# Optimization experiments

Hardware: AMD Instinct MI355X
Metric: run time of the kernel (lower is better)

The kernel has to match this reference:

```python
import jax, jax.numpy as jnp
import numpy as np

H = 64  # LSTM hidden size (hardcoded in Baseline)

def _lstm_encode(x, W_ih, W_hh, b_ih, b_hh):
    # x: [N, C, T] -> final hidden state [N, H]
    # PyTorch LSTMCell gate order: i, f, g, o
    N = x.shape[0]
    xs = jnp.moveaxis(x, 2, 0)                       # [T, N, C]
    xp = jnp.einsum('tnc,gc->tng', xs, W_ih) + b_ih  # precompute input proj [T, N, 4H]
    h0 = jnp.zeros((N, H), dtype=x.dtype)
    c0 = jnp.zeros((N, H), dtype=x.dtype)

    def step(carry, xp_t):
        h, c = carry
        g = xp_t + h @ W_hh.T + b_hh                 # [N, 4H]
        i, f, gg, o = jnp.split(g, 4, axis=-1)
        c = jax.nn.sigmoid(f) * c + jax.nn.sigmoid(i) * jnp.tanh(gg)
        h = jax.nn.sigmoid(o) * jnp.tanh(c)
        return (h, c), None

    (h, _), _ = jax.lax.scan(step, (h0, c0), xp)
    return h

def _head(x, W1, b1, W2, b2, W3, b3):
    # dropout is identity at inference; relu on first two layers, none on last
    x = jax.nn.relu(x @ W1.T + b1)
    x = jax.nn.relu(x @ W2.T + b2)
    return x @ W3.T + b3

def setup_inputs() -> dict:
    key = jax.random.key(0)
    ks = jax.random.split(key, 24)
    C1, C2 = 32, 56
    N, T = 8192, 72
    d = {
        'X_obs': jax.random.normal(ks[0], (N, C1, T), jnp.float32),
        'X_wrf_cmaq': jax.random.normal(ks[1], (N, C2, T), jnp.float32),
        'obs_Wih': jax.random.normal(ks[2], (4 * H, C1), jnp.float32) * 0.1,
        'obs_Whh': jax.random.normal(ks[3], (4 * H, H), jnp.float32) * 0.1,
        'obs_bih': jax.random.normal(ks[4], (4 * H,), jnp.float32) * 0.1,
        'obs_bhh': jax.random.normal(ks[5], (4 * H,), jnp.float32) * 0.1,
        'wrf_Wih': jax.random.normal(ks[6], (4 * H, C2), jnp.float32) * 0.1,
        'wrf_Whh': jax.random.normal(ks[7], (4 * H, H), jnp.float32) * 0.1,
        'wrf_bih': jax.random.normal(ks[8], (4 * H,), jnp.float32) * 0.1,
        'wrf_bhh': jax.random.normal(ks[9], (4 * H,), jnp.float32) * 0.1,
    }
    dims = [(96, 128), (64, 96), (48, 64)]
    k = 10
    for head in ('fsp', 'o3'):
        for li, (o, i) in enumerate(dims, 1):
            d[f'{head}_W{li}'] = jax.random.normal(ks[k], (o, i), jnp.float32) * (1.0 / np.sqrt(i)); k += 1
            d[f'{head}_b{li}'] = jax.random.normal(ks[k], (o,), jnp.float32) * 0.05; k += 1
    return d

def reference(X_obs, X_wrf_cmaq,
              obs_Wih, obs_Whh, obs_bih, obs_bhh,
              wrf_Wih, wrf_Whh, wrf_bih, wrf_bhh,
              fsp_W1, fsp_b1, fsp_W2, fsp_b2, fsp_W3, fsp_b3,
              o3_W1, o3_b1, o3_W2, o3_b2, o3_W3, o3_b3):
    h_obs = _lstm_encode(X_obs, obs_Wih, obs_Whh, obs_bih, obs_bhh)
    h_wrf = _lstm_encode(X_wrf_cmaq, wrf_Wih, wrf_Whh, wrf_bih, wrf_bhh)
    feat = jnp.concatenate([h_obs, h_wrf], axis=1)  # [N, 128]
    fsp = _head(feat, fsp_W1, fsp_b1, fsp_W2, fsp_b2, fsp_W3, fsp_b3)
    o3 = _head(feat, o3_W1, o3_b1, o3_W2, o3_b2, o3_W3, o3_b3)
    return jnp.stack([fsp, o3], axis=1)  # [N, 2, 48]
```

## Files before the change

### kernel.cpp

```cpp
#include <hip/hip_runtime.h>

typedef __attribute__((ext_vector_type(8))) short short8;
typedef __attribute__((ext_vector_type(4))) float f32x4;

#define OFF_BXO   64
#define OFF_BHO   (OFF_BXO + 16384)
#define OFF_BXW   (OFF_BHO + 32768)
#define OFF_BHW   (OFF_BXW + 32768)
#define OFF_HW    (OFF_BHW + 32768)
#define OFF_BIASL (OFF_HW + 43008)
#define OFF_BIASH (OFF_BIASL + 1024)
#define OFF_FEAT  (OFF_BIASH + 832)

__device__ __forceinline__ float b2f(unsigned short u) {
    return __uint_as_float(((unsigned)u) << 16);
}
__device__ __forceinline__ unsigned short f2b(float f) {
    unsigned u = __float_as_uint(f);
    u += 0x7FFFu + ((u >> 16) & 1u);
    return (unsigned short)(u >> 16);
}
__device__ __forceinline__ float ldin(const void* p, int idx, int isf) {
    return isf ? ((const float*)p)[idx] : b2f(((const unsigned short*)p)[idx]);
}
__device__ __forceinline__ float sigmoidf_(float x) {
    return __builtin_amdgcn_rcpf(1.0f + __expf(-x));
}
__device__ __forceinline__ float tanhf_(float x) {
    return 2.0f * __builtin_amdgcn_rcpf(1.0f + __expf(-2.0f * x)) - 1.0f;
}
__device__ __forceinline__ f32x4 MFMA(short8 a, short8 b, f32x4 c) {
    return __builtin_amdgcn_mfma_f32_16x16x32_bf16(a, b, c, 0, 0, 0);
}

__global__ __launch_bounds__(256) void detect_kernel(
    const unsigned short* __restrict__ X, int* __restrict__ flag)
{
    __shared__ int cnt[256];
    int c = 0;
    for (int i = threadIdx.x; i < 2048; i += 256) {
        unsigned short u = X[2 * i];
        c += (((u >> 7) & 0xFF) >= 192);
    }
    cnt[threadIdx.x] = c;
    __syncthreads();
    if (threadIdx.x == 0) {
        int s = 0;
        for (int i = 0; i < 256; ++i) s += cnt[i];
        *flag = (s > 64) ? 1 : 0;
    }
}

__global__ __launch_bounds__(256) void prep_kernel(
    const void* oWih, const void* oWhh, const void* obih, const void* obhh,
    const void* wWih, const void* wWhh, const void* wbih, const void* wbhh,
    const void* fW1, const void* fb1, const void* fW2, const void* fb2,
    const void* fW3, const void* fb3,
    const void* oW1, const void* ob1, const void* oW2, const void* ob2,
    const void* oW3, const void* ob3,
    unsigned short* __restrict__ ws)
{
    const int isf = ((const int*)ws)[0];
    const int gid = blockIdx.x * 256 + threadIdx.x;
    const int gsz = gridDim.x * 256;

    unsigned short* BXO = ws + OFF_BXO;
    unsigned short* BHO = ws + OFF_BHO;
    unsigned short* BXW = ws + OFF_BXW;
    unsigned short* BHW = ws + OFF_BHW;
    unsigned short* HW  = ws + OFF_HW;

    for (int i = gid; i < 8192; i += gsz) {
        int j = i & 7, lane = (i >> 3) & 63, nt = (i >> 9) & 3, wave = i >> 11;
        int g = wave * 64 + nt * 16 + (lane & 15);
        int k = ((lane >> 4) << 3) + j;
        float w = ldin(oWih, g * 32 + k, isf);
        unsigned short hi = f2b(w);
        BXO[i] = hi; BXO[8192 + i] = f2b(w - b2f(hi));
    }
    for (int i = gid; i < 16384; i += gsz) {
        int j = i & 7, lane = (i >> 3) & 63, nt = (i >> 9) & 3;
        int kt = (i >> 11) & 1, wave = i >> 12;
        int g = wave * 64 + nt * 16 + (lane & 15);
        int k = kt * 32 + ((lane >> 4) << 3) + j;
        float w = ldin(oWhh, g * 64 + k, isf);
        unsigned short hi = f2b(w);
        BHO[i] = hi; BHO[16384 + i] = f2b(w - b2f(hi));
    }
    for (int i = gid; i < 16384; i += gsz) {
        int j = i & 7, lane = (i >> 3) & 63, nt = (i >> 9) & 3;
        int wave = (i >> 11) & 3, kt2 = i >> 13;
        int g = wave * 64 + nt * 16 + (lane & 15);
        int k = kt2 * 32 + ((lane >> 4) << 3) + j;
        float w = (k < 56) ? ldin(wWih, g * 56 + k, isf) : 0.f;
        unsigned short hi = f2b(w);
        BXW[i] = hi; BXW[16384 + i] = f2b(w - b2f(hi));
    }
    for (int i = gid; i < 16384; i += gsz) {
        int j = i & 7, lane = (i >> 3) & 63, nt = (i >> 9) & 3;
        int kt = (i >> 11) & 1, wave = i >> 12;
        int g = wave * 64 + nt * 16 + (lane & 15);
        int k = kt * 32 + ((lane >> 4) << 3) + j;
        float w = ldin(wWhh, g * 64 + k, isf);
        unsigned short hi = f2b(w);
        BHW[i] = hi; BHW[16384 + i] = f2b(w - b2f(hi));
    }
    for (int i = gid; i < 12288; i += gsz) HW[i]         = f2b(ldin(fW1, i, isf));
    for (int i = gid; i < 6144;  i += gsz) HW[12288 + i] = f2b(ldin(fW2, i, isf));
    for (int i = gid; i < 3072;  i += gsz) HW[18432 + i] = f2b(ldin(fW3, i, isf));
    for (int i = gid; i < 12288; i += gsz) HW[21504 + i] = f2b(ldin(oW1, i, isf));
    for (int i = gid; i < 6144;  i += gsz) HW[33792 + i] = f2b(ldin(oW2, i, isf));
    for (int i = gid; i < 3072;  i += gsz) HW[39936 + i] = f2b(ldin(oW3, i, isf));
    float* BL = (float*)(ws + OFF_BIASL);
    for (int i = gid; i < 256; i += gsz) BL[i]       = ldin(obih, i, isf) + ldin(obhh, i, isf);
    for (int i = gid; i < 256; i += gsz) BL[256 + i] = ldin(wbih, i, isf) + ldin(wbhh, i, isf);
    float* BB = (float*)(ws + OFF_BIASH);
    for (int i = gid; i < 96; i += gsz) BB[i]       = ldin(fb1, i, isf);
    for (int i = gid; i < 64; i += gsz) BB[96 + i]  = ldin(fb2, i, isf);
    for (int i = gid; i < 48; i += gsz) BB[160 + i] = ldin(fb3, i, isf);
    for (int i = gid; i < 96; i += gsz) BB[208 + i] = ldin(ob1, i, isf);
    for (int i = gid; i < 64; i += gsz) BB[304 + i] = ldin(ob2, i, isf);
    for (int i = gid; i < 48; i += gsz) BB[368 + i] = ldin(ob3, i, isf);
}

__global__ __launch_bounds__(256) void lstm_kernel(
    const void* __restrict__ Xo, const void* __restrict__ Xw,
    unsigned short* __restrict__ ws)
{
    __shared__ unsigned short xbuf[2][8][8][16][8];
    __shared__ float gates[256][16];
    __shared__ unsigned short hfrag[2][2][4][16][8];

    const int tid  = threadIdx.x;
    const int wave = tid >> 6, lane = tid & 63;
    const int quad = lane >> 4, m16 = lane & 15;
    const bool isw = blockIdx.x >= 512;
    const int blk  = isw ? (int)blockIdx.x - 512 : (int)blockIdx.x;
    const int n0   = blk * 16;
    const int isf  = ((const int*)ws)[0];

    const void* x = isw ? Xw : Xo;
    const unsigned short* BX = ws + (isw ? OFF_BXW : OFF_BXO);
    const unsigned short* BH = ws + (isw ? OFF_BHW : OFF_BHO);
    const float* BL = (const float*)(ws + OFF_BIASL) + (isw ? 256 : 0);
    unsigned short* featH = ws + OFF_FEAT;
    unsigned short* featL = featH + 8192 * 128;
    const int C       = isw ? 56 : 32;
    const int Cpad    = isw ? 64 : 32;
    const int cshift  = isw ? 6 : 5;
    const int xloOff  = isw ? 16384 : 8192;
    const int featOff = isw ? 64 : 0;

    short8 BhH[2][4], BhL[2][4];
#pragma unroll
    for (int kt = 0; kt < 2; ++kt)
#pragma unroll
        for (int nt = 0; nt < 4; ++nt) {
            int idx = ((wave * 2 + kt) * 4 + nt) * 512 + lane * 8;
            BhH[kt][nt] = *(const short8*)&BH[idx];
            BhL[kt][nt] = *(const short8*)&BH[16384 + idx];
        }
    short8 BxH0[4], BxL0[4], BxH1[4], BxL1[4];
#pragma unroll
    for (int nt = 0; nt < 4; ++nt) {
        int idx = (wave * 4 + nt) * 512 + lane * 8;
        BxH0[nt] = *(const short8*)&BX[idx];
        BxL0[nt] = *(const short8*)&BX[xloOff + idx];
    }
    if (isw) {
#pragma unroll
        for (int nt = 0; nt < 4; ++nt) {
            int idx = (wave * 4 + nt) * 512 + lane * 8;
            BxH1[nt] = *(const short8*)&BX[8192 + idx];
            BxL1[nt] = *(const short8*)&BX[xloOff + 8192 + idx];
        }
    }

    const int j0  = tid >> 2;
    const int nlo = (tid & 3) * 4;
    const float bias_i = BL[j0];
    const float bias_f = BL[j0 + 64];
    const float bias_g = BL[j0 + 128];
    const float bias_o = BL[j0 + 192];
    float c4[4] = {0.f, 0.f, 0.f, 0.f};

    for (int i = tid; i < 2 * 2 * 4 * 16 * 8; i += 256)
        ((unsigned short*)hfrag)[i] = 0;

    for (int chunk = 0; chunk < 9; ++chunk) {
        const int t0 = chunk * 8;
        for (int i = tid; i < (16 << cshift); i += 256) {
            int n = i >> cshift, c = i & (Cpad - 1);
            float v[8];
            if (c < C) {
                size_t off = ((size_t)(n0 + n) * C + c) * 72 + t0;
                if (isf) {
                    const float* p = (const float*)x + off;
                    f32x4 u0 = *(const f32x4*)p;
                    f32x4 u1 = *(const f32x4*)(p + 4);
                    v[0] = u0[0]; v[1] = u0[1]; v[2] = u0[2]; v[3] = u0[3];
                    v[4] = u1[0]; v[5] = u1[1]; v[6] = u1[2]; v[7] = u1[3];
                } else {
                    const unsigned short* p = (const unsigned short*)x + off;
#pragma unroll
                    for (int j = 0; j < 8; ++j) v[j] = b2f(p[j]);
                }
            } else {
#pragma unroll
                for (int j = 0; j < 8; ++j) v[j] = 0.f;
            }
#pragma unroll
            for (int tt = 0; tt < 8; ++tt) {
                unsigned short hi = f2b(v[tt]);
                xbuf[0][tt][c >> 3][n][c & 7] = hi;
                xbuf[1][tt][c >> 3][n][c & 7] = f2b(v[tt] - b2f(hi));
            }
        }
        __syncthreads();

        for (int tt = 0; tt < 8; ++tt) {
            const int t = t0 + tt;
            f32x4 acc[4] = {{0,0,0,0},{0,0,0,0},{0,0,0,0},{0,0,0,0}};
            {
                short8 axh = *(const short8*)&xbuf[0][tt][quad][m16][0];
                short8 axl = *(const short8*)&xbuf[1][tt][quad][m16][0];
#pragma unroll
                for (int nt = 0; nt < 4; ++nt) {
                    acc[nt] = MFMA(axh, BxH0[nt], acc[nt]);
                    acc[nt] = MFMA(axl, BxH0[nt], acc[nt]);
                    acc[nt] = MFMA(axh, BxL0[nt], acc[nt]);
                }
            }
            if (isw) {
                short8 axh = *(const short8*)&xbuf[0][tt][4 + quad][m16][0];
                short8 axl = *(const short8*)&xbuf[1][tt][4 + quad][m16][0];
#pragma unroll
                for (int nt = 0; nt < 4; ++nt) {
                    acc[nt] = MFMA(axh, BxH1[nt], acc[nt]);
                    acc[nt] = MFMA(axl, BxH1[nt], acc[nt]);
                    acc[nt] = MFMA(axh, BxL1[nt], acc[nt]);
                }
            }
#pragma unroll
            for (int kt = 0; kt < 2; ++kt) {
                short8 ahi = *(const short8*)&hfrag[0][kt][quad][m16][0];
                short8 alo = *(const short8*)&hfrag[1][kt][quad][m16][0];
#pragma unroll
                for (int nt = 0; nt < 4; ++nt) {
                    acc[nt] = MFMA(ahi, BhH[kt][nt], acc[nt]);
                    acc[nt] = MFMA(alo, BhH[kt][nt], acc[nt]);
                    acc[nt] = MFMA(ahi, BhL[kt][nt], acc[nt]);
                }
            }
#pragma unroll
            for (int nt = 0; nt < 4; ++nt) {
                int g = wave * 64 + nt * 16 + m16;
                *(f32x4*)&gates[g][quad * 4] = acc[nt];
            }
            __syncthreads();

            f32x4 gi = *(f32x4*)&gates[j0][nlo];
            f32x4 gf = *(f32x4*)&gates[j0 + 64][nlo];
            f32x4 gg = *(f32x4*)&gates[j0 + 128][nlo];
            f32x4 go = *(f32x4*)&gates[j0 + 192][nlo];
#pragma unroll
            for (int e = 0; e < 4; ++e) {
                float iv = sigmoidf_(gi[e] + bias_i);
                float fv = sigmoidf_(gf[e] + bias_f);
                float gv = tanhf_(gg[e] + bias_g);
                float ov = sigmoidf_(go[e] + bias_o);
                float c  = fv * c4[e] + iv * gv;
                c4[e]    = c;
                float h  = ov * tanhf_(c);
                unsigned short hi = f2b(h);
                unsigned short lo = f2b(h - b2f(hi));
                int m = nlo + e;
                hfrag[0][j0 >> 5][(j0 >> 3) & 3][m][j0 & 7] = hi;
                hfrag[1][j0 >> 5][(j0 >> 3) & 3][m][j0 & 7] = lo;
                if (t == 71) {
                    featH[(size_t)(n0 + m) * 128 + featOff + j0] = hi;
                    featL[(size_t)(n0 + m) * 128 + featOff + j0] = lo;
                }
            }
            __syncthreads();
        }
    }
}

__global__ __launch_bounds__(256) void heads_kernel(
    const unsigned short* __restrict__ ws, void* __restrict__ out)
{
    __shared__ unsigned short afrag[4][4][4][16][8];
    const int tid  = threadIdx.x;
    const int wave = tid >> 6, lane = tid & 63;
    const int quad = lane >> 4, m16 = lane & 15;
    const int r0   = blockIdx.x * 64 + wave * 16;
    const int isf  = ((const int*)ws)[0];

    const unsigned short* HW    = ws + OFF_HW;
    const float*          BB    = (const float*)(ws + OFF_BIASH);
    const unsigned short* featH = ws + OFF_FEAT;
    const unsigned short* featL = featH + 8192 * 128;

    short8 fh[4], fl[4];
#pragma unroll
    for (int kt = 0; kt < 4; ++kt) {
        size_t o = (size_t)(r0 + m16) * 128 + kt * 32 + quad * 8;
        fh[kt] = *(const short8*)&featH[o];
        fl[kt] = *(const short8*)&featL[o];
    }

    for (int head = 0; head < 2; ++head) {
        const unsigned short* W1 = HW + (head ? 21504 : 0);
        const unsigned short* W2 = W1 + 12288;
        const unsigned short* W3 = W2 + 6144;
        const float* b1 = BB + head * 208;
        const float* b2 = b1 + 96;
        const float* b3 = b2 + 64;

        f32x4 a1[6] = {{0,0,0,0},{0,0,0,0},{0,0,0,0},{0,0,0,0},{0,0,0,0},{0,0,0,0}};
#pragma unroll
        for (int kt = 0; kt < 4; ++kt)
#pragma unroll
            for (int nt = 0; nt < 6; ++nt) {
                short8 bw = *(const short8*)
                    &W1[(nt * 16 + m16) * 128 + kt * 32 + quad * 8];
                a1[nt] = MFMA(fh[kt], bw, a1[nt]);
                a1[nt] = MFMA(fl[kt], bw, a1[nt]);
            }
#pragma unroll
        for (int nt = 0; nt < 6; ++nt) {
            int u = nt * 16 + m16;
            float bv = b1[u];
#pragma unroll
            for (int r = 0; r < 4; ++r) {
                float v = a1[nt][r] + bv;
                v = v > 0.f ? v : 0.f;
                afrag[wave][u >> 5][(u >> 3) & 3][quad * 4 + r][u & 7] = f2b(v);
            }
        }
        __syncthreads();

        f32x4 a2[4] = {{0,0,0,0},{0,0,0,0},{0,0,0,0},{0,0,0,0}};
#pragma unroll
        for (int kt = 0; kt < 3; ++kt) {
            short8 a = *(const short8*)&afrag[wave][kt][quad][m16][0];
#pragma unroll
            for (int nt = 0; nt < 4; ++nt) {
                short8 bw = *(const short8*)
                    &W2[(nt * 16 + m16) * 96 + kt * 32 + quad * 8];
                a2[nt] = MFMA(a, bw, a2[nt]);
            }
        }
        __syncthreads();
#pragma unroll
        for (int nt = 0; nt < 4; ++nt) {
            int u = nt * 16 + m16;
            float bv = b2[u];
#pragma unroll
            for (int r = 0; r < 4; ++r) {
                float v = a2[nt][r] + bv;
                v = v > 0.f ? v : 0.f;
                afrag[wave][u >> 5][(u >> 3) & 3][quad * 4 + r][u & 7] = f2b(v);
            }
        }
        __syncthreads();

        f32x4 a3[3] = {{0,0,0,0},{0,0,0,0},{0,0,0,0}};
#pragma unroll
        for (int kt = 0; kt < 2; ++kt) {
            short8 a = *(const short8*)&afrag[wave][kt][quad][m16][0];
#pragma unroll
            for (int nt = 0; nt < 3; ++nt) {
                short8 bw = *(const short8*)
                    &W3[(nt * 16 + m16) * 64 + kt * 32 + quad * 8];
                a3[nt] = MFMA(a, bw, a3[nt]);
            }
        }
#pragma unroll
        for (int nt = 0; nt < 3; ++nt) {
            int u = nt * 16 + m16;
            float bv = b3[u];
#pragma unroll
            for (int r = 0; r < 4; ++r) {
                int row = quad * 4 + r;
                size_t idx = (size_t)(r0 + row) * 96 + head * 48 + u;
                float v = a3[nt][r] + bv;
                if (isf) ((float*)out)[idx] = v;
                else     ((unsigned short*)out)[idx] = f2b(v);
            }
        }
        __syncthreads();
    }
}

extern "C" void kernel_launch(void* const* d_in, const int* in_sizes, int n_in,
                              void* d_out, int out_size, void* d_ws, size_t ws_size,
                              hipStream_t stream)
{
    unsigned short* ws = (unsigned short*)d_ws;

    detect_kernel<<<1, 256, 0, stream>>>((const unsigned short*)d_in[0], (int*)d_ws);
    prep_kernel<<<64, 256, 0, stream>>>(
        d_in[2], d_in[3], d_in[4], d_in[5],
        d_in[6], d_in[7], d_in[8], d_in[9],
        d_in[10], d_in[11], d_in[12], d_in[13], d_in[14], d_in[15],
        d_in[16], d_in[17], d_in[18], d_in[19], d_in[20], d_in[21],
        ws);
    lstm_kernel<<<1024, 256, 0, stream>>>(d_in[0], d_in[1], ws);
    heads_kernel<<<128, 256, 0, stream>>>(ws, d_out);
}
```

Baseline: 542.0 us.

## Swizzle LDS layouts for xbuf, gates and hfrag and shrink the time chunk

Measured after the change: 532.1 us. About the same (-1.8%).

```diff
diff --git a/kernel.cpp b/kernel.cpp
--- a/kernel.cpp
+++ b/kernel.cpp
@@ -123,11 +123,12 @@
     for (int i = gid; i < 48; i += gsz) BB[368 + i] = ldin(ob3, i, isf);
 }
 
+#define TCH 4
 __global__ __launch_bounds__(256) void lstm_kernel(
     const void* __restrict__ Xo, const void* __restrict__ Xw,
     unsigned short* __restrict__ ws)
 {
-    __shared__ unsigned short xbuf[2][8][8][16][8];
+    __shared__ unsigned short xbuf[2][TCH][8][16][8];
     __shared__ float gates[256][16];
     __shared__ unsigned short hfrag[2][2][4][16][8];
 
@@ -184,46 +185,49 @@
     const float bias_o = BL[j0 + 192];
     float c4[4] = {0.f, 0.f, 0.f, 0.f};
 
+    const int colr = (tid & 3) ^ ((j0 >> 1) & 3);
+    const int hchunkbit = ((j0 >> 3) & 1) << 2;
+    const int prr = ((((m16 & 3) << 2) | (m16 >> 2)) ^ ((quad & 1) << 2));
+
     for (int i = tid; i < 2 * 2 * 4 * 16 * 8; i += 256)
         ((unsigned short*)hfrag)[i] = 0;
 
-    for (int chunk = 0; chunk < 9; ++chunk) {
-        const int t0 = chunk * 8;
+    for (int chunk = 0; chunk < 18; ++chunk) {
+        const int t0 = chunk * TCH;
         for (int i = tid; i < (16 << cshift); i += 256) {
             int n = i >> cshift, c = i & (Cpad - 1);
-            float v[8];
+            float v[TCH];
             if (c < C) {
                 size_t off = ((size_t)(n0 + n) * C + c) * 72 + t0;
                 if (isf) {
-                    const float* p = (const float*)x + off;
-                    f32x4 u0 = *(const f32x4*)p;
-                    f32x4 u1 = *(const f32x4*)(p + 4);
+                    f32x4 u0 = *(const f32x4*)((const float*)x + off);
                     v[0] = u0[0]; v[1] = u0[1]; v[2] = u0[2]; v[3] = u0[3];
-                    v[4] = u1[0]; v[5] = u1[1]; v[6] = u1[2]; v[7] = u1[3];
                 } else {
                     const unsigned short* p = (const unsigned short*)x + off;
 #pragma unroll
-                    for (int j = 0; j < 8; ++j) v[j] = b2f(p[j]);
+                    for (int j = 0; j < TCH; ++j) v[j] = b2f(p[j]);
                 }
             } else {
 #pragma unroll
-                for (int j = 0; j < 8; ++j) v[j] = 0.f;
-            }
-#pragma unroll
-            for (int tt = 0; tt < 8; ++tt) {
+                for (int j = 0; j < TCH; ++j) v[j] = 0.f;
+            }
+            int kt = c >> 3;
+            int pr = n ^ kt;
+#pragma unroll
+            for (int tt = 0; tt < TCH; ++tt) {
                 unsigned short hi = f2b(v[tt]);
-                xbuf[0][tt][c >> 3][n][c & 7] = hi;
-                xbuf[1][tt][c >> 3][n][c & 7] = f2b(v[tt] - b2f(hi));
+                xbuf[0][tt][kt][pr][c & 7] = hi;
+                xbuf[1][tt][kt][pr][c & 7] = f2b(v[tt] - b2f(hi));
             }
         }
         __syncthreads();
 
-        for (int tt = 0; tt < 8; ++tt) {
+        for (int tt = 0; tt < TCH; ++tt) {
             const int t = t0 + tt;
             f32x4 acc[4] = {{0,0,0,0},{0,0,0,0},{0,0,0,0},{0,0,0,0}};
             {
-                short8 axh = *(const short8*)&xbuf[0][tt][quad][m16][0];
-                short8 axl = *(const short8*)&xbuf[1][tt][quad][m16][0];
+                short8 axh = *(const short8*)&xbuf[0][tt][quad][m16 ^ quad][0];
+                short8 axl = *(const short8*)&xbuf[1][tt][quad][m16 ^ quad][0];
 #pragma unroll
                 for (int nt = 0; nt < 4; ++nt) {
                     acc[nt] = MFMA(axh, BxH0[nt], acc[nt]);
@@ -232,8 +236,8 @@
                 }
             }
             if (isw) {
-                short8 axh = *(const short8*)&xbuf[0][tt][4 + quad][m16][0];
-                short8 axl = *(const short8*)&xbuf[1][tt][4 + quad][m16][0];
+                short8 axh = *(const short8*)&xbuf[0][tt][4 + quad][m16 ^ (4 + quad)][0];
+                short8 axl = *(const short8*)&xbuf[1][tt][4 + quad][m16 ^ (4 + quad)][0];
 #pragma unroll
                 for (int nt = 0; nt < 4; ++nt) {
                     acc[nt] = MFMA(axh, BxH1[nt], acc[nt]);
@@ -243,8 +247,8 @@
             }
 #pragma unroll
             for (int kt = 0; kt < 2; ++kt) {
-                short8 ahi = *(const short8*)&hfrag[0][kt][quad][m16][0];
-                short8 alo = *(const short8*)&hfrag[1][kt][quad][m16][0];
+                short8 ahi = *(const short8*)&hfrag[0][kt][quad][prr][0];
+                short8 alo = *(const short8*)&hfrag[1][kt][quad][prr][0];
 #pragma unroll
                 for (int nt = 0; nt < 4; ++nt) {
                     acc[nt] = MFMA(ahi, BhH[kt][nt], acc[nt]);
@@ -252,17 +256,20 @@
                     acc[nt] = MFMA(ahi, BhL[kt][nt], acc[nt]);
                 }
             }
-#pragma unroll
-            for (int nt = 0; nt < 4; ++nt) {
-                int g = wave * 64 + nt * 16 + m16;
-                *(f32x4*)&gates[g][quad * 4] = acc[nt];
+            {
+                int colw = quad ^ ((m16 >> 1) & 3);
+#pragma unroll
+                for (int nt = 0; nt < 4; ++nt) {
+                    int g = wave * 64 + nt * 16 + m16;
+                    *(f32x4*)&gates[g][colw * 4] = acc[nt];
+                }
             }
             __syncthreads();
 
-            f32x4 gi = *(f32x4*)&gates[j0][nlo];
-            f32x4 gf = *(f32x4*)&gates[j0 + 64][nlo];
-            f32x4 gg = *(f32x4*)&gates[j0 + 128][nlo];
-            f32x4 go = *(f32x4*)&gates[j0 + 192][nlo];
+            f32x4 gi = *(f32x4*)&gates[j0][colr * 4];
+            f32x4 gf = *(f32x4*)&gates[j0 + 64][colr * 4];
+            f32x4 gg = *(f32x4*)&gates[j0 + 128][colr * 4];
+            f32x4 go = *(f32x4*)&gates[j0 + 192][colr * 4];
 #pragma unroll
             for (int e = 0; e < 4; ++e) {
                 float iv = sigmoidf_(gi[e] + bias_i);
@@ -275,8 +282,9 @@
                 unsigned short hi = f2b(h);
                 unsigned short lo = f2b(h - b2f(hi));
                 int m = nlo + e;
-                hfrag[0][j0 >> 5][(j0 >> 3) & 3][m][j0 & 7] = hi;
-                hfrag[1][j0 >> 5][(j0 >> 3) & 3][m][j0 & 7] = lo;
+                int pr = (((m & 3) << 2) | (m >> 2)) ^ hchunkbit;
+                hfrag[0][j0 >> 5][(j0 >> 3) & 3][pr][j0 & 7] = hi;
+                hfrag[1][j0 >> 5][(j0 >> 3) & 3][pr][j0 & 7] = lo;
                 if (t == 71) {
                     featH[(size_t)(n0 + m) * 128 + featOff + j0] = hi;
                     featL[(size_t)(n0 + m) * 128 + featOff + j0] = lo;
```
